# Optimization experiments

Hardware: AMD Instinct MI355X
Metric: run time of the kernel (lower is better)

Reference implementation:

```python
import jax, jax.numpy as jnp
import numpy as np

N, E, F_NODE, F_EDGE, EMB, HID, NGRAPH = 10000, 30000, 32, 8, 64, 16, 64


def _edge_mlp(e, w1, b1, w2, b2):
    # Seq(Linear(F_EDGE,16), ReLU, Linear(16, in*out))
    return jax.nn.relu(e @ w1 + b1) @ w2 + b2


def setup_inputs() -> dict:
    key = jax.random.key(0)
    ks = jax.random.split(key, 24)
    s = lambda k, shape, fan: jax.random.normal(k, shape, jnp.float32) * (1.0 / np.sqrt(fan))
    inp = {
        "x_p": jax.random.normal(ks[0], (N, F_NODE), jnp.float32),
        "x_d": jax.random.normal(ks[1], (1, F_NODE), jnp.float32),
        "edge_attr_p": jax.random.uniform(ks[2], (E, F_EDGE), jnp.float32),
        "edge_attr_d": jax.random.uniform(ks[3], (1, F_EDGE), jnp.float32),
        "edge_index_p": jax.random.randint(ks[4], (2, E), 0, N, jnp.int32),
        "x_p_batch": jnp.sort(jax.random.randint(ks[5], (N,), 0, NGRAPH, jnp.int32)),
        # edge MLP of first conv: F_EDGE -> 16 -> F_NODE*EMB
        "nn0_w1": s(ks[6], (F_EDGE, HID), F_EDGE), "nn0_b1": jnp.zeros((HID,), jnp.float32),
        "nn0_w2": s(ks[7], (HID, F_NODE * EMB), HID), "nn0_b2": jnp.zeros((F_NODE * EMB,), jnp.float32),
        # shared edge MLP of later convs: F_EDGE -> 16 -> EMB*EMB
        "nn1_w1": s(ks[8], (F_EDGE, HID), F_EDGE), "nn1_b1": jnp.zeros((HID,), jnp.float32),
        "nn1_w2": s(ks[9], (HID, EMB * EMB), HID), "nn1_b2": jnp.zeros((EMB * EMB,), jnp.float32),
        # per-conv root weights and biases
        "root0": s(ks[10], (F_NODE, EMB), F_NODE), "bias0": jnp.zeros((EMB,), jnp.float32),
        "root1": s(ks[11], (EMB, EMB), EMB), "bias1": jnp.zeros((EMB,), jnp.float32),
        "root2": s(ks[12], (EMB, EMB), EMB), "bias2": jnp.zeros((EMB,), jnp.float32),
        # head: Linear(EMB,EMB) then Linear(EMB,1), no activation between (per source)
        "lin0_w": s(ks[13], (EMB, EMB), EMB), "lin0_b": jnp.zeros((EMB,), jnp.float32),
        "lin1_w": s(ks[14], (EMB, 1), EMB), "lin1_b": jnp.zeros((1,), jnp.float32),
    }
    return inp


def reference(x_p, x_d, edge_attr_p, edge_attr_d,
              nn0_w1, nn0_b1, nn0_w2, nn0_b2,
              nn1_w1, nn1_b1, nn1_w2, nn1_b2,
              root0, bias0, root1, bias1, root2, bias2,
              lin0_w, lin0_b, lin1_w, lin1_b,
              edge_index_p, x_p_batch):
    src, dst = edge_index_p[0], edge_index_p[1]

    # conv 0: edge-conditioned weights [E, F_NODE, EMB]
    W0 = _edge_mlp(edge_attr_p, nn0_w1, nn0_b1, nn0_w2, nn0_b2).reshape(E, F_NODE, EMB)
    msg = jnp.einsum('ei,eio->eo', x_p[src], W0)
    agg = jax.ops.segment_sum(msg, dst, num_segments=N)
    x = jax.nn.relu(agg + x_p @ root0 + bias0)

    # convs 1..L-1 share the same edge MLP (same nn1 instance in source), so
    # the per-edge weight matrices [E, EMB, EMB] are identical: compute once.
    W1 = _edge_mlp(edge_attr_p, nn1_w1, nn1_b1, nn1_w2, nn1_b2).reshape(E, EMB, EMB)
    for root, bias in ((root1, bias1), (root2, bias2)):
        msg = jnp.einsum('ei,eio->eo', x[src], W1)
        agg = jax.ops.segment_sum(msg, dst, num_segments=N)
        x = jax.nn.relu(agg + x @ root + bias)

    # global max pool over graphs, dropout is identity in eval mode
    pooled = jax.ops.segment_max(x, x_p_batch, num_segments=NGRAPH)
    h = pooled @ lin0_w + lin0_b
    out = h @ lin1_w + lin1_b  # [NGRAPH, 1]
    return out
```

## Files before the change

kernel.cpp:

```cpp
#include <hip/hip_runtime.h>
#include <hip/hip_bf16.h>

#define N_NODES 10000
#define N_EDGES 30000
#define F_NODE  32
#define F_EDGE  8
#define EMB     64
#define HID     16
#define NGRAPH  64
#define NBUCK   625
#define CAP     128
#define NCOL    1088
#define ROWW    514

typedef __attribute__((ext_vector_type(8))) short short8;
typedef __attribute__((ext_vector_type(4))) float f32x4;

__device__ __forceinline__ unsigned short f2b(float f) {
    __hip_bfloat16 h = __float2bfloat16(f);
    return __builtin_bit_cast(unsigned short, h);
}

struct P {
    const float *x_p, *ea;
    const int *src, *dst, *batch;
    const float *nn0_w1, *nn0_b1, *nn0_w2, *nn0_b2;
    const float *nn1_w1, *nn1_b1, *nn1_w2, *nn1_b2;
    const float *root0, *bias0, *root1, *bias1, *root2, *bias2;
    const float *lin0_w, *lin0_b, *lin1_w, *lin1_b;
    float *out;
    int *cnt, *metap;
    float *A1p;
    unsigned short *W2p0, *W2p1;
    float *AGGa, *AGGb, *X0, *X1, *POOL;
};

__global__ void __launch_bounds__(256) k_prep(P p) {
    int b = blockIdx.x, t = threadIdx.x;
    if (b < 136) {
        int i = b * 256 + t;
        if (i >= NCOL * F_NODE) return;
        int rt = i >> 5, k = i & 31;
        float v;
        if (rt < 1024) {
            int T = rt >> 4, lr = rt & 15;
            int o = ((T >> 4) << 4) + lr, h = T & 15;
            v = p.nn0_w2[h * (F_NODE * EMB) + k * EMB + o];
        } else {
            v = p.nn0_b2[k * EMB + (rt - 1024)];
        }
        p.W2p0[i] = f2b(v);
    } else if (b < 408) {
        int i = (b - 136) * 256 + t;
        if (i >= NCOL * EMB) return;
        int rt = i >> 6, k = i & 63;
        float v;
        if (rt < 1024) {
            int T = rt >> 4, lr = rt & 15;
            int o = ((T >> 4) << 4) + lr, h = T & 15;
            v = p.nn1_w2[h * (EMB * EMB) + k * EMB + o];
        } else {
            v = p.nn1_b2[k * EMB + (rt - 1024)];
        }
        p.W2p1[i] = f2b(v);
    } else {
        int idx = (b - 408) * 256 + t;
        float4* Z = (float4*)p.AGGa;
        const float4 z4 = {0.f, 0.f, 0.f, 0.f};
        const int nv4 = (N_NODES * EMB + NGRAPH * EMB) / 4;
        for (int i = idx; i < nv4; i += 160 * 256) Z[i] = z4;
    }
}

template <int CONV>
__global__ void __launch_bounds__(512) k_fused(P p) {
    constexpr int K = (CONV == 0) ? F_NODE : EMB;
    __shared__ unsigned short U2[16 * 2 * ROWW];
    __shared__ float XB_l[16][65];
    __shared__ float Xt[16][65];
    __shared__ float A0l[CAP][HID];
    __shared__ int lds_e[CAP];
    __shared__ int meta_l[CAP];
    __shared__ int lcnt;
    const int b = blockIdx.x, t = threadIdx.x;
    const int n0 = b * 16;
    const int w = t >> 6, l = t & 63;
    const int lrow = l & 15, lk4 = l >> 4;
    int cnt = 0;

    if (CONV == 0) {
        float4* Zb = (float4*)(p.AGGb + (size_t)n0 * EMB);
        const float4 z4 = {0.f, 0.f, 0.f, 0.f};
        for (int idx = t; idx < 16 * EMB / 4; idx += 512) Zb[idx] = z4;
        if (t == 0) lcnt = 0;
        __syncthreads();
        const int4* s4 = (const int4*)p.src;
        for (int i = t; i < N_EDGES / 4; i += 512) {
            int4 v = s4[i];
            int e0 = i * 4;
            if ((v.x >> 4) == b) { int sl = atomicAdd(&lcnt, 1); if (sl < CAP) lds_e[sl] = ((e0    ) << 4) | (v.x & 15); }
            if ((v.y >> 4) == b) { int sl = atomicAdd(&lcnt, 1); if (sl < CAP) lds_e[sl] = ((e0 + 1) << 4) | (v.y & 15); }
            if ((v.z >> 4) == b) { int sl = atomicAdd(&lcnt, 1); if (sl < CAP) lds_e[sl] = ((e0 + 2) << 4) | (v.z & 15); }
            if ((v.w >> 4) == b) { int sl = atomicAdd(&lcnt, 1); if (sl < CAP) lds_e[sl] = ((e0 + 3) << 4) | (v.w & 15); }
        }
        __syncthreads();
        cnt = lcnt; if (cnt > CAP) cnt = CAP;
        if (t == 0) p.cnt[b] = cnt;
        if (t < cnt) {
            int pk = lds_e[t];
            int e = pk >> 4, sloc = pk & 15;
            int mt = p.dst[e] * 16 + sloc;
            meta_l[t] = mt;
            p.metap[(size_t)b * CAP + t] = mt;
            const float4* ea4 = (const float4*)(p.ea + (size_t)e * F_EDGE);
            float4 ef0 = ea4[0], ef1 = ea4[1];
            float fv[F_EDGE] = {ef0.x, ef0.y, ef0.z, ef0.w, ef1.x, ef1.y, ef1.z, ef1.w};
            float a1v[HID];
#pragma unroll
            for (int h = 0; h < HID; h++) {
                float s0 = p.nn0_b1[h], s1 = p.nn1_b1[h];
#pragma unroll
                for (int i = 0; i < F_EDGE; i++) {
                    s0 += fv[i] * p.nn0_w1[i * HID + h];
                    s1 += fv[i] * p.nn1_w1[i * HID + h];
                }
                A0l[t][h] = fmaxf(s0, 0.f);
                a1v[h] = fmaxf(s1, 0.f);
            }
            float4* A1g = (float4*)(p.A1p + ((size_t)b * CAP + t) * HID);
#pragma unroll
            for (int j = 0; j < 4; j++)
                A1g[j] = float4{a1v[4 * j], a1v[4 * j + 1], a1v[4 * j + 2], a1v[4 * j + 3]};
        }
    }

    if (CONV > 0) {
        const float* aggIn = (CONV == 1) ? p.AGGa : p.AGGb;
        const float* rt = (CONV == 1) ? p.root0 : p.root1;
        const float* bs = (CONV == 1) ? p.bias0 : p.bias1;
        constexpr int IN = (CONV == 1) ? F_NODE : EMB;
        for (int idx = t; idx < 16 * 64; idx += 512) {
            int j = idx >> 6, o = idx & 63;
            int n = n0 + j;
            float s = aggIn[n * EMB + o] + bs[o];
            const float* xr = (CONV == 1) ? (p.x_p + (size_t)n * IN)
                                          : (p.X0 + (size_t)n * IN);
#pragma unroll
            for (int i = 0; i < IN; i++) s += xr[i] * rt[i * EMB + o];
            float sv = fmaxf(s, 0.f);
            Xt[j][o] = sv;
            if (CONV == 1) { p.X0[n * EMB + o] = sv; p.AGGa[n * EMB + o] = 0.f; }
            else           { p.X1[n * EMB + o] = sv; }
        }
        __syncthreads();
        cnt = p.cnt[b];
    }

    short8 afr[K / 32];
    if (CONV == 0) {
        const float* xp = p.x_p + (size_t)(n0 + lrow) * F_NODE + lk4 * 8;
#pragma unroll
        for (int q = 0; q < 8; q++) afr[0][q] = (short)f2b(xp[q]);
    } else {
#pragma unroll
        for (int kk = 0; kk < K / 32; kk++)
#pragma unroll
            for (int q = 0; q < 8; q++)
                afr[kk][q] = (short)f2b(Xt[lrow][kk * 32 + lk4 * 8 + q]);
    }
    const unsigned short* W2p = (CONV == 0) ? p.W2p0 : p.W2p1;
    for (int i = 0; i <= 8; i++) {
        int T = w + 8 * i;
        if (T >= 68) break;
        short8 bfr[K / 32];
#pragma unroll
        for (int kk = 0; kk < K / 32; kk++)
            bfr[kk] = *reinterpret_cast<const short8*>(
                W2p + (size_t)(T * 16 + lrow) * K + kk * 32 + lk4 * 8);
        f32x4 acc = {0.f, 0.f, 0.f, 0.f};
#pragma unroll
        for (int kk = 0; kk < K / 32; kk++)
            acc = __builtin_amdgcn_mfma_f32_16x16x32_bf16(afr[kk], bfr[kk], acc, 0, 0, 0);
        if (T < 64) {
            int h = T & 15, hw = h >> 1, hb = h & 1;
            int ob = ((T >> 4) << 4) + lrow;
#pragma unroll
            for (int r = 0; r < 4; r++)
                U2[(lk4 * 4 + r) * (2 * ROWW) + hw * 128 + ob * 2 + hb] = f2b(acc[r]);
        } else {
            int col = (T - 64) * 16 + lrow;
#pragma unroll
            for (int r = 0; r < 4; r++)
                XB_l[lk4 * 4 + r][col] = acc[r];
        }
    }
    __syncthreads();

    float* aggOut = (CONV == 1) ? p.AGGb : p.AGGa;
    const size_t base = (size_t)b * CAP;
    const int o = l;
#pragma unroll 2
    for (int qi = w; qi < cnt; qi += 8) {
        int q = __builtin_amdgcn_readfirstlane(qi);
        int mt;
        float av[HID];
        if (CONV == 0) {
            mt = meta_l[q];
            const float4* a4 = (const float4*)A0l[q];
            float4 u0 = a4[0], u1 = a4[1], u2 = a4[2], u3 = a4[3];
            av[0]=u0.x; av[1]=u0.y; av[2]=u0.z; av[3]=u0.w;
            av[4]=u1.x; av[5]=u1.y; av[6]=u1.z; av[7]=u1.w;
            av[8]=u2.x; av[9]=u2.y; av[10]=u2.z; av[11]=u2.w;
            av[12]=u3.x; av[13]=u3.y; av[14]=u3.z; av[15]=u3.w;
        } else {
            mt = p.metap[base + q];
            const float* Ae = p.A1p + (base + q) * HID;
#pragma unroll
            for (int h = 0; h < HID; h++) av[h] = Ae[h];
        }
        int sloc = mt & 15, dd = mt >> 4;
        const unsigned* up = reinterpret_cast<const unsigned*>(U2) + sloc * ROWW + o;
        float m = XB_l[sloc][o];
#define ACC2(wrd, h)                                                              \
        m = fmaf(__builtin_bit_cast(float, (unsigned)(wrd) << 16), av[h], m);     \
        m = fmaf(__builtin_bit_cast(float, (unsigned)(wrd) & 0xffff0000u), av[h + 1], m);
#pragma unroll
        for (int hh = 0; hh < 8; hh++) {
            unsigned uw = up[hh * 64];
            ACC2(uw, 2 * hh)
        }
#undef ACC2
        atomicAdd(&aggOut[(size_t)dd * EMB + o], m);
    }
}

__global__ void __launch_bounds__(256) k_upd2(P p) {
    int w = threadIdx.x >> 6, o = threadIdx.x & 63;
    int n = __builtin_amdgcn_readfirstlane(blockIdx.x * 4 + w);
    float s = p.AGGa[n * EMB + o] + p.bias2[o];
    const float* xr = p.X1 + (size_t)n * EMB;
#pragma unroll
    for (int i = 0; i < EMB; i++) s += xr[i] * p.root2[i * EMB + o];
    s = fmaxf(s, 0.f);
    atomicMax((unsigned*)&p.POOL[p.batch[n] * EMB + o], __float_as_uint(s));
}

__global__ void k_head(P p) {
    int g = blockIdx.x, o2 = threadIdx.x;
    float h = p.lin0_b[o2];
    const float* Pg = p.POOL + g * EMB;
    for (int o = 0; o < EMB; o++) h += Pg[o] * p.lin0_w[o * EMB + o2];
    float v = h * p.lin1_w[o2];
#pragma unroll
    for (int off = 32; off; off >>= 1) v += __shfl_down(v, off, 64);
    if (o2 == 0) p.out[g] = v + p.lin1_b[0];
}

extern "C" void kernel_launch(void* const* d_in, const int* in_sizes, int n_in,
                              void* d_out, int out_size, void* d_ws, size_t ws_size,
                              hipStream_t stream) {
    P p;
    p.x_p    = (const float*)d_in[0];
    p.ea     = (const float*)d_in[2];
    const int* eidx = (const int*)d_in[4];
    p.src    = eidx;
    p.dst    = eidx + N_EDGES;
    p.batch  = (const int*)d_in[5];
    p.nn0_w1 = (const float*)d_in[6];  p.nn0_b1 = (const float*)d_in[7];
    p.nn0_w2 = (const float*)d_in[8];  p.nn0_b2 = (const float*)d_in[9];
    p.nn1_w1 = (const float*)d_in[10]; p.nn1_b1 = (const float*)d_in[11];
    p.nn1_w2 = (const float*)d_in[12]; p.nn1_b2 = (const float*)d_in[13];
    p.root0  = (const float*)d_in[14]; p.bias0  = (const float*)d_in[15];
    p.root1  = (const float*)d_in[16]; p.bias1  = (const float*)d_in[17];
    p.root2  = (const float*)d_in[18]; p.bias2  = (const float*)d_in[19];
    p.lin0_w = (const float*)d_in[20]; p.lin0_b = (const float*)d_in[21];
    p.lin1_w = (const float*)d_in[22]; p.lin1_b = (const float*)d_in[23];
    p.out    = (float*)d_out;

    char* ws = (char*)d_ws;
    p.AGGa   = (float*)ws;
    p.POOL   = p.AGGa + (size_t)N_NODES * EMB;
    char* w2 = (char*)(p.POOL + (size_t)NGRAPH * EMB);
    p.AGGb   = (float*)w2;          w2 += (size_t)N_NODES * EMB * 4;
    p.cnt    = (int*)w2;            w2 += 2560;
    p.metap  = (int*)w2;            w2 += (size_t)NBUCK * CAP * 4;
    p.A1p    = (float*)w2;          w2 += (size_t)NBUCK * CAP * HID * 4;
    p.W2p0   = (unsigned short*)w2; w2 += (size_t)NCOL * F_NODE * 2;
    p.W2p1   = (unsigned short*)w2; w2 += (size_t)NCOL * EMB * 2;
    p.X0     = (float*)w2;          w2 += (size_t)N_NODES * EMB * 4;
    p.X1     = (float*)w2;          w2 += (size_t)N_NODES * EMB * 4;

    k_prep<<<568, 256, 0, stream>>>(p);
    k_fused<0><<<NBUCK, 512, 0, stream>>>(p);
    k_fused<1><<<NBUCK, 512, 0, stream>>>(p);
    k_fused<2><<<NBUCK, 512, 0, stream>>>(p);
    k_upd2<<<2500, 256, 0, stream>>>(p);
    k_head<<<NGRAPH, 64, 0, stream>>>(p);
}
```

Before: 203.3 us.

## Replace global atomic scatter with per-edge message buffers and bucketed gather

Each conv now writes per-edge messages to a dense buffer instead of atomically adding into the global node aggregate. The next stage gathers incoming messages per destination bucket into LDS using shared-memory atomics, which removes the zeroing passes and the global float atomics. The separate prep kernel is dropped; the bf16 weight packing is now done inline from the fp32 weights inside each fused kernel, with strided global loads. In exchange there is extra global traffic for the per-edge message buffers and redundant weight conversion in every block.

```diff
diff --git a/kernel.cpp b/kernel.cpp
--- a/kernel.cpp
+++ b/kernel.cpp
@@ -10,7 +10,6 @@
 #define NGRAPH  64
 #define NBUCK   625
 #define CAP     128
-#define NCOL    1088
 #define ROWW    514
 
 typedef __attribute__((ext_vector_type(8))) short short8;
@@ -29,48 +28,10 @@
     const float *root0, *bias0, *root1, *bias1, *root2, *bias2;
     const float *lin0_w, *lin0_b, *lin1_w, *lin1_b;
     float *out;
-    int *cnt, *metap;
+    int *cnt, *dcnt, *metap, *dstm;
     float *A1p;
-    unsigned short *W2p0, *W2p1;
-    float *AGGa, *AGGb, *X0, *X1, *POOL;
+    float *MSGa, *MSGb, *X0, *X1, *POOL;
 };
-
-__global__ void __launch_bounds__(256) k_prep(P p) {
-    int b = blockIdx.x, t = threadIdx.x;
-    if (b < 136) {
-        int i = b * 256 + t;
-        if (i >= NCOL * F_NODE) return;
-        int rt = i >> 5, k = i & 31;
-        float v;
-        if (rt < 1024) {
-            int T = rt >> 4, lr = rt & 15;
-            int o = ((T >> 4) << 4) + lr, h = T & 15;
-            v = p.nn0_w2[h * (F_NODE * EMB) + k * EMB + o];
-        } else {
-            v = p.nn0_b2[k * EMB + (rt - 1024)];
-        }
-        p.W2p0[i] = f2b(v);
-    } else if (b < 408) {
-        int i = (b - 136) * 256 + t;
-        if (i >= NCOL * EMB) return;
-        int rt = i >> 6, k = i & 63;
-        float v;
-        if (rt < 1024) {
-            int T = rt >> 4, lr = rt & 15;
-            int o = ((T >> 4) << 4) + lr, h = T & 15;
-            v = p.nn1_w2[h * (EMB * EMB) + k * EMB + o];
-        } else {
-            v = p.nn1_b2[k * EMB + (rt - 1024)];
-        }
-        p.W2p1[i] = f2b(v);
-    } else {
-        int idx = (b - 408) * 256 + t;
-        float4* Z = (float4*)p.AGGa;
-        const float4 z4 = {0.f, 0.f, 0.f, 0.f};
-        const int nv4 = (N_NODES * EMB + NGRAPH * EMB) / 4;
-        for (int i = idx; i < nv4; i += 160 * 256) Z[i] = z4;
-    }
-}
 
 template <int CONV>
 __global__ void __launch_bounds__(512) k_fused(P p) {
@@ -80,38 +41,41 @@
     __shared__ float Xt[16][65];
     __shared__ float A0l[CAP][HID];
     __shared__ int lds_e[CAP];
-    __shared__ int meta_l[CAP];
-    __shared__ int lcnt;
+    __shared__ int lds_d[CAP];
+    __shared__ int lcs, lcd;
     const int b = blockIdx.x, t = threadIdx.x;
     const int n0 = b * 16;
     const int w = t >> 6, l = t & 63;
     const int lrow = l & 15, lk4 = l >> 4;
-    int cnt = 0;
+    int scnt = 0;
 
     if (CONV == 0) {
-        float4* Zb = (float4*)(p.AGGb + (size_t)n0 * EMB);
-        const float4 z4 = {0.f, 0.f, 0.f, 0.f};
-        for (int idx = t; idx < 16 * EMB / 4; idx += 512) Zb[idx] = z4;
-        if (t == 0) lcnt = 0;
+        int gtid = b * 512 + t;
+        if (gtid < (NGRAPH * EMB) / 4)
+            ((float4*)p.POOL)[gtid] = float4{0.f, 0.f, 0.f, 0.f};
+        if (t == 0) { lcs = 0; lcd = 0; }
         __syncthreads();
         const int4* s4 = (const int4*)p.src;
+        const int4* d4 = (const int4*)p.dst;
         for (int i = t; i < N_EDGES / 4; i += 512) {
-            int4 v = s4[i];
+            int4 sv = s4[i];
+            int4 dv = d4[i];
             int e0 = i * 4;
-            if ((v.x >> 4) == b) { int sl = atomicAdd(&lcnt, 1); if (sl < CAP) lds_e[sl] = ((e0    ) << 4) | (v.x & 15); }
-            if ((v.y >> 4) == b) { int sl = atomicAdd(&lcnt, 1); if (sl < CAP) lds_e[sl] = ((e0 + 1) << 4) | (v.y & 15); }
-            if ((v.z >> 4) == b) { int sl = atomicAdd(&lcnt, 1); if (sl < CAP) lds_e[sl] = ((e0 + 2) << 4) | (v.z & 15); }
-            if ((v.w >> 4) == b) { int sl = atomicAdd(&lcnt, 1); if (sl < CAP) lds_e[sl] = ((e0 + 3) << 4) | (v.w & 15); }
-        }
-        __syncthreads();
-        cnt = lcnt; if (cnt > CAP) cnt = CAP;
-        if (t == 0) p.cnt[b] = cnt;
-        if (t < cnt) {
+#define CHK(sx, dx, eo)                                                                           \
+            if (((sx) >> 4) == b) { int sl = atomicAdd(&lcs, 1); if (sl < CAP) lds_e[sl] = (((e0) + (eo)) << 4) | ((sx) & 15); } \
+            if (((dx) >> 4) == b) { int sl = atomicAdd(&lcd, 1); if (sl < CAP) lds_d[sl] = (((e0) + (eo)) << 4) | ((dx) & 15); }
+            CHK(sv.x, dv.x, 0) CHK(sv.y, dv.y, 1) CHK(sv.z, dv.z, 2) CHK(sv.w, dv.w, 3)
+#undef CHK
+        }
+        __syncthreads();
+        scnt = lcs; if (scnt > CAP) scnt = CAP;
+        int dcv = lcd; if (dcv > CAP) dcv = CAP;
+        if (t == 0) { p.cnt[b] = scnt; p.dcnt[b] = dcv; }
+        if (t < dcv) p.dstm[(size_t)b * CAP + t] = lds_d[t];
+        if (t < scnt) {
             int pk = lds_e[t];
-            int e = pk >> 4, sloc = pk & 15;
-            int mt = p.dst[e] * 16 + sloc;
-            meta_l[t] = mt;
-            p.metap[(size_t)b * CAP + t] = mt;
+            int e = pk >> 4;
+            p.metap[(size_t)b * CAP + t] = pk;
             const float4* ea4 = (const float4*)(p.ea + (size_t)e * F_EDGE);
             float4 ef0 = ea4[0], ef1 = ea4[1];
             float fv[F_EDGE] = {ef0.x, ef0.y, ef0.z, ef0.w, ef1.x, ef1.y, ef1.z, ef1.w};
@@ -135,25 +99,35 @@
     }
 
     if (CONV > 0) {
-        const float* aggIn = (CONV == 1) ? p.AGGa : p.AGGb;
+        int dcv = p.dcnt[b];
+        for (int idx = t; idx < 16 * 64; idx += 512) Xt[idx >> 6][idx & 63] = 0.f;
+        __syncthreads();
+        const float* MSGin = (CONV == 1) ? p.MSGa : p.MSGb;
+        for (int jj = w; jj < dcv; jj += 8) {
+            int q = __builtin_amdgcn_readfirstlane(jj);
+            int mt = p.dstm[(size_t)b * CAP + q];
+            int e = mt >> 4, dloc = mt & 15;
+            atomicAdd(&Xt[dloc][l], MSGin[(size_t)e * EMB + l]);
+        }
+        __syncthreads();
         const float* rt = (CONV == 1) ? p.root0 : p.root1;
         const float* bs = (CONV == 1) ? p.bias0 : p.bias1;
         constexpr int IN = (CONV == 1) ? F_NODE : EMB;
         for (int idx = t; idx < 16 * 64; idx += 512) {
             int j = idx >> 6, o = idx & 63;
             int n = n0 + j;
-            float s = aggIn[n * EMB + o] + bs[o];
+            float s = Xt[j][o] + bs[o];
             const float* xr = (CONV == 1) ? (p.x_p + (size_t)n * IN)
                                           : (p.X0 + (size_t)n * IN);
 #pragma unroll
             for (int i = 0; i < IN; i++) s += xr[i] * rt[i * EMB + o];
             float sv = fmaxf(s, 0.f);
             Xt[j][o] = sv;
-            if (CONV == 1) { p.X0[n * EMB + o] = sv; p.AGGa[n * EMB + o] = 0.f; }
-            else           { p.X1[n * EMB + o] = sv; }
-        }
-        __syncthreads();
-        cnt = p.cnt[b];
+            if (CONV == 1) p.X0[n * EMB + o] = sv;
+            else           p.X1[n * EMB + o] = sv;
+        }
+        __syncthreads();
+        scnt = p.cnt[b];
     }
 
     short8 afr[K / 32];
@@ -168,15 +142,28 @@
             for (int q = 0; q < 8; q++)
                 afr[kk][q] = (short)f2b(Xt[lrow][kk * 32 + lk4 * 8 + q]);
     }
-    const unsigned short* W2p = (CONV == 0) ? p.W2p0 : p.W2p1;
     for (int i = 0; i <= 8; i++) {
         int T = w + 8 * i;
         if (T >= 68) break;
         short8 bfr[K / 32];
-#pragma unroll
-        for (int kk = 0; kk < K / 32; kk++)
-            bfr[kk] = *reinterpret_cast<const short8*>(
-                W2p + (size_t)(T * 16 + lrow) * K + kk * 32 + lk4 * 8);
+        if (T < 64) {
+            int h = T & 15, ob = ((T >> 4) << 4) + lrow;
+            const float* wb = (CONV == 0) ? (p.nn0_w2 + (size_t)h * (F_NODE * EMB) + ob)
+                                          : (p.nn1_w2 + (size_t)h * (EMB * EMB) + ob);
+#pragma unroll
+            for (int kk = 0; kk < K / 32; kk++)
+#pragma unroll
+                for (int q = 0; q < 8; q++)
+                    bfr[kk][q] = (short)f2b(wb[(size_t)(kk * 32 + lk4 * 8 + q) * EMB]);
+        } else {
+            int col = (T - 64) * 16 + lrow;
+            const float* bb = (CONV == 0) ? (p.nn0_b2 + col) : (p.nn1_b2 + col);
+#pragma unroll
+            for (int kk = 0; kk < K / 32; kk++)
+#pragma unroll
+                for (int q = 0; q < 8; q++)
+                    bfr[kk][q] = (short)f2b(bb[(size_t)(kk * 32 + lk4 * 8 + q) * EMB]);
+        }
         f32x4 acc = {0.f, 0.f, 0.f, 0.f};
 #pragma unroll
         for (int kk = 0; kk < K / 32; kk++)
@@ -196,16 +183,16 @@
     }
     __syncthreads();
 
-    float* aggOut = (CONV == 1) ? p.AGGb : p.AGGa;
+    float* MSGout = (CONV == 1) ? p.MSGb : p.MSGa;
     const size_t base = (size_t)b * CAP;
     const int o = l;
 #pragma unroll 2
-    for (int qi = w; qi < cnt; qi += 8) {
+    for (int qi = w; qi < scnt; qi += 8) {
         int q = __builtin_amdgcn_readfirstlane(qi);
         int mt;
         float av[HID];
         if (CONV == 0) {
-            mt = meta_l[q];
+            mt = lds_e[q];
             const float4* a4 = (const float4*)A0l[q];
             float4 u0 = a4[0], u1 = a4[1], u2 = a4[2], u3 = a4[3];
             av[0]=u0.x; av[1]=u0.y; av[2]=u0.z; av[3]=u0.w;
@@ -218,7 +205,7 @@
 #pragma unroll
             for (int h = 0; h < HID; h++) av[h] = Ae[h];
         }
-        int sloc = mt & 15, dd = mt >> 4;
+        int e = mt >> 4, sloc = mt & 15;
         const unsigned* up = reinterpret_cast<const unsigned*>(U2) + sloc * ROWW + o;
         float m = XB_l[sloc][o];
 #define ACC2(wrd, h)                                                              \
@@ -230,19 +217,35 @@
             ACC2(uw, 2 * hh)
         }
 #undef ACC2
-        atomicAdd(&aggOut[(size_t)dd * EMB + o], m);
-    }
-}
-
-__global__ void __launch_bounds__(256) k_upd2(P p) {
-    int w = threadIdx.x >> 6, o = threadIdx.x & 63;
-    int n = __builtin_amdgcn_readfirstlane(blockIdx.x * 4 + w);
-    float s = p.AGGa[n * EMB + o] + p.bias2[o];
-    const float* xr = p.X1 + (size_t)n * EMB;
-#pragma unroll
-    for (int i = 0; i < EMB; i++) s += xr[i] * p.root2[i * EMB + o];
-    s = fmaxf(s, 0.f);
-    atomicMax((unsigned*)&p.POOL[p.batch[n] * EMB + o], __float_as_uint(s));
+        MSGout[(size_t)e * EMB + o] = m;
+    }
+}
+
+__global__ void __launch_bounds__(512) k_upd2(P p) {
+    __shared__ float Xt[16][65];
+    const int b = blockIdx.x, t = threadIdx.x;
+    const int n0 = b * 16;
+    const int w = t >> 6, l = t & 63;
+    int dcv = p.dcnt[b];
+    for (int idx = t; idx < 16 * 64; idx += 512) Xt[idx >> 6][idx & 63] = 0.f;
+    __syncthreads();
+    for (int jj = w; jj < dcv; jj += 8) {
+        int q = __builtin_amdgcn_readfirstlane(jj);
+        int mt = p.dstm[(size_t)b * CAP + q];
+        int e = mt >> 4, dloc = mt & 15;
+        atomicAdd(&Xt[dloc][l], p.MSGa[(size_t)e * EMB + l]);
+    }
+    __syncthreads();
+    for (int idx = t; idx < 16 * 64; idx += 512) {
+        int j = idx >> 6, o = idx & 63;
+        int n = n0 + j;
+        float s = Xt[j][o] + p.bias2[o];
+        const float* xr = p.X1 + (size_t)n * EMB;
+#pragma unroll
+        for (int i = 0; i < EMB; i++) s += xr[i] * p.root2[i * EMB + o];
+        s = fmaxf(s, 0.f);
+        atomicMax((unsigned*)&p.POOL[p.batch[n] * EMB + o], __float_as_uint(s));
+    }
 }
 
 __global__ void k_head(P p) {
@@ -278,22 +281,20 @@
     p.out    = (float*)d_out;
 
     char* ws = (char*)d_ws;
-    p.AGGa   = (float*)ws;
-    p.POOL   = p.AGGa + (size_t)N_NODES * EMB;
-    char* w2 = (char*)(p.POOL + (size_t)NGRAPH * EMB);
-    p.AGGb   = (float*)w2;          w2 += (size_t)N_NODES * EMB * 4;
-    p.cnt    = (int*)w2;            w2 += 2560;
-    p.metap  = (int*)w2;            w2 += (size_t)NBUCK * CAP * 4;
-    p.A1p    = (float*)w2;          w2 += (size_t)NBUCK * CAP * HID * 4;
-    p.W2p0   = (unsigned short*)w2; w2 += (size_t)NCOL * F_NODE * 2;
-    p.W2p1   = (unsigned short*)w2; w2 += (size_t)NCOL * EMB * 2;
-    p.X0     = (float*)w2;          w2 += (size_t)N_NODES * EMB * 4;
-    p.X1     = (float*)w2;          w2 += (size_t)N_NODES * EMB * 4;
-
-    k_prep<<<568, 256, 0, stream>>>(p);
+    p.cnt   = (int*)ws;            ws += 2560;
+    p.dcnt  = (int*)ws;            ws += 2560;
+    p.metap = (int*)ws;            ws += (size_t)NBUCK * CAP * 4;
+    p.dstm  = (int*)ws;            ws += (size_t)NBUCK * CAP * 4;
+    p.A1p   = (float*)ws;          ws += (size_t)NBUCK * CAP * HID * 4;
+    p.MSGa  = (float*)ws;          ws += (size_t)N_EDGES * EMB * 4;
+    p.MSGb  = (float*)ws;          ws += (size_t)N_EDGES * EMB * 4;
+    p.X0    = (float*)ws;          ws += (size_t)N_NODES * EMB * 4;
+    p.X1    = (float*)ws;          ws += (size_t)N_NODES * EMB * 4;
+    p.POOL  = (float*)ws;          ws += (size_t)NGRAPH * EMB * 4;
+
     k_fused<0><<<NBUCK, 512, 0, stream>>>(p);
     k_fused<1><<<NBUCK, 512, 0, stream>>>(p);
     k_fused<2><<<NBUCK, 512, 0, stream>>>(p);
-    k_upd2<<<2500, 256, 0, stream>>>(p);
+    k_upd2<<<NBUCK, 512, 0, stream>>>(p);
     k_head<<<NGRAPH, 64, 0, stream>>>(p);
 }
```

New measurement: 241.9 us. 19.0% more time.

## Fuse final node update, max-pool and head into one per-graph kernel

Applied to the files above, without the earlier changes.

Replaces the final node-update kernel (2500 blocks with global atomicMax into a POOL buffer) and the separate head kernel with a single per-graph kernel. Each block binary-searches the sorted batch array for its node range, does the root2 update, pools in LDS, then applies the linear head. This removes one launch, the global pool buffer and its zeroing, and the global atomics. It also splits the bf16 FMA chain in the conv kernels into two accumulators for more ILP. The trade-off is that only 64 blocks cover all 10000 nodes, so the tail runs with little parallelism.

```diff
diff --git a/kernel.cpp b/kernel.cpp
--- a/kernel.cpp
+++ b/kernel.cpp
@@ -32,7 +32,7 @@
     int *cnt, *metap;
     float *A1p;
     unsigned short *W2p0, *W2p1;
-    float *AGGa, *AGGb, *X0, *X1, *POOL;
+    float *AGGa, *AGGb, *X0, *X1;
 };
 
 __global__ void __launch_bounds__(256) k_prep(P p) {
@@ -67,8 +67,7 @@
         int idx = (b - 408) * 256 + t;
         float4* Z = (float4*)p.AGGa;
         const float4 z4 = {0.f, 0.f, 0.f, 0.f};
-        const int nv4 = (N_NODES * EMB + NGRAPH * EMB) / 4;
-        for (int i = idx; i < nv4; i += 160 * 256) Z[i] = z4;
+        for (int i = idx; i < (N_NODES * EMB) / 4; i += 160 * 256) Z[i] = z4;
     }
 }
 
@@ -220,40 +219,54 @@
         }
         int sloc = mt & 15, dd = mt >> 4;
         const unsigned* up = reinterpret_cast<const unsigned*>(U2) + sloc * ROWW + o;
-        float m = XB_l[sloc][o];
-#define ACC2(wrd, h)                                                              \
-        m = fmaf(__builtin_bit_cast(float, (unsigned)(wrd) << 16), av[h], m);     \
-        m = fmaf(__builtin_bit_cast(float, (unsigned)(wrd) & 0xffff0000u), av[h + 1], m);
-#pragma unroll
-        for (int hh = 0; hh < 8; hh++) {
-            unsigned uw = up[hh * 64];
-            ACC2(uw, 2 * hh)
+        float m0 = XB_l[sloc][o], m1 = 0.f;
+#define ACC2(dst_, wrd, h)                                                            \
+        dst_ = fmaf(__builtin_bit_cast(float, (unsigned)(wrd) << 16), av[h], dst_);   \
+        dst_ = fmaf(__builtin_bit_cast(float, (unsigned)(wrd) & 0xffff0000u), av[h + 1], dst_);
+#pragma unroll
+        for (int hh = 0; hh < 4; hh++) {
+            unsigned ua = up[hh * 64];
+            unsigned ub = up[(hh + 4) * 64];
+            ACC2(m0, ua, 2 * hh)
+            ACC2(m1, ub, 2 * (hh + 4))
         }
 #undef ACC2
-        atomicAdd(&aggOut[(size_t)dd * EMB + o], m);
-    }
-}
-
-__global__ void __launch_bounds__(256) k_upd2(P p) {
-    int w = threadIdx.x >> 6, o = threadIdx.x & 63;
-    int n = __builtin_amdgcn_readfirstlane(blockIdx.x * 4 + w);
-    float s = p.AGGa[n * EMB + o] + p.bias2[o];
-    const float* xr = p.X1 + (size_t)n * EMB;
-#pragma unroll
-    for (int i = 0; i < EMB; i++) s += xr[i] * p.root2[i * EMB + o];
-    s = fmaxf(s, 0.f);
-    atomicMax((unsigned*)&p.POOL[p.batch[n] * EMB + o], __float_as_uint(s));
-}
-
-__global__ void k_head(P p) {
-    int g = blockIdx.x, o2 = threadIdx.x;
-    float h = p.lin0_b[o2];
-    const float* Pg = p.POOL + g * EMB;
-    for (int o = 0; o < EMB; o++) h += Pg[o] * p.lin0_w[o * EMB + o2];
-    float v = h * p.lin1_w[o2];
-#pragma unroll
-    for (int off = 32; off; off >>= 1) v += __shfl_down(v, off, 64);
-    if (o2 == 0) p.out[g] = v + p.lin1_b[0];
+        atomicAdd(&aggOut[(size_t)dd * EMB + o], m0 + m1);
+    }
+}
+
+__global__ void __launch_bounds__(256) k_tail(P p) {
+    __shared__ unsigned pool[EMB];
+    const int g = blockIdx.x, t = threadIdx.x;
+    const int w = t >> 6, o = t & 63;
+    if (t < EMB) pool[t] = 0u;
+    __syncthreads();
+    int lo = 0, hi = N_NODES;
+    while (lo < hi) { int mid = (lo + hi) >> 1; if (p.batch[mid] < g) lo = mid + 1; else hi = mid; }
+    int lo2 = lo, hi2 = N_NODES;
+    while (lo2 < hi2) { int mid = (lo2 + hi2) >> 1; if (p.batch[mid] < g + 1) lo2 = mid + 1; else hi2 = mid; }
+    const float b2 = p.bias2[o];
+    for (int n0 = lo + w; n0 < lo2; n0 += 4) {
+        int n = __builtin_amdgcn_readfirstlane(n0);
+        float s = p.AGGa[(size_t)n * EMB + o] + b2;
+        const float* xr = p.X1 + (size_t)n * EMB;
+#pragma unroll
+        for (int i = 0; i < EMB; i++) s += xr[i] * p.root2[i * EMB + o];
+        s = fmaxf(s, 0.f);
+        atomicMax(&pool[o], __float_as_uint(s));
+    }
+    __syncthreads();
+    if (t < EMB) {
+        int o2 = t;
+        float h = p.lin0_b[o2];
+#pragma unroll 8
+        for (int oo = 0; oo < EMB; oo++)
+            h += __uint_as_float(pool[oo]) * p.lin0_w[oo * EMB + o2];
+        float v = h * p.lin1_w[o2];
+#pragma unroll
+        for (int off = 32; off; off >>= 1) v += __shfl_down(v, off, 64);
+        if (o2 == 0) p.out[g] = v + p.lin1_b[0];
+    }
 }
 
 extern "C" void kernel_launch(void* const* d_in, const int* in_sizes, int n_in,
@@ -278,22 +291,19 @@
     p.out    = (float*)d_out;
 
     char* ws = (char*)d_ws;
-    p.AGGa   = (float*)ws;
-    p.POOL   = p.AGGa + (size_t)N_NODES * EMB;
-    char* w2 = (char*)(p.POOL + (size_t)NGRAPH * EMB);
-    p.AGGb   = (float*)w2;          w2 += (size_t)N_NODES * EMB * 4;
-    p.cnt    = (int*)w2;            w2 += 2560;
-    p.metap  = (int*)w2;            w2 += (size_t)NBUCK * CAP * 4;
-    p.A1p    = (float*)w2;          w2 += (size_t)NBUCK * CAP * HID * 4;
-    p.W2p0   = (unsigned short*)w2; w2 += (size_t)NCOL * F_NODE * 2;
-    p.W2p1   = (unsigned short*)w2; w2 += (size_t)NCOL * EMB * 2;
-    p.X0     = (float*)w2;          w2 += (size_t)N_NODES * EMB * 4;
-    p.X1     = (float*)w2;          w2 += (size_t)N_NODES * EMB * 4;
+    p.AGGa   = (float*)ws;          ws += (size_t)N_NODES * EMB * 4;
+    p.AGGb   = (float*)ws;          ws += (size_t)N_NODES * EMB * 4;
+    p.cnt    = (int*)ws;            ws += 2560;
+    p.metap  = (int*)ws;            ws += (size_t)NBUCK * CAP * 4;
+    p.A1p    = (float*)ws;          ws += (size_t)NBUCK * CAP * HID * 4;
+    p.W2p0   = (unsigned short*)ws; ws += (size_t)NCOL * F_NODE * 2;
+    p.W2p1   = (unsigned short*)ws; ws += (size_t)NCOL * EMB * 2;
+    p.X0     = (float*)ws;          ws += (size_t)N_NODES * EMB * 4;
+    p.X1     = (float*)ws;          ws += (size_t)N_NODES * EMB * 4;
 
     k_prep<<<568, 256, 0, stream>>>(p);
     k_fused<0><<<NBUCK, 512, 0, stream>>>(p);
     k_fused<1><<<NBUCK, 512, 0, stream>>>(p);
     k_fused<2><<<NBUCK, 512, 0, stream>>>(p);
-    k_upd2<<<2500, 256, 0, stream>>>(p);
-    k_head<<<NGRAPH, 64, 0, stream>>>(p);
-}
+    k_tail<<<NGRAPH, 256, 0, stream>>>(p);
+}
```

Measured after the change: 214.7 us. 5.6% more time.
